# Optimization experiments

Measured on AMD Instinct MI355X. Metric: run time of the kernel, lower is better.

## Reference

```python
import jax, jax.numpy as jnp
import numpy as np

T, B, I, H, O = 256, 64, 512, 1024, 256


def setup_inputs() -> dict:
    key = jax.random.key(0)
    ks = jax.random.split(key, 7)
    s_ih = 1.0 / np.sqrt(H)
    return {
        "x": jax.random.normal(ks[0], (T, B, I), dtype=jnp.float32),
        "W_ih": jax.random.uniform(ks[1], (4 * H, I), dtype=jnp.float32, minval=-s_ih, maxval=s_ih),
        "W_hh": jax.random.uniform(ks[2], (4 * H, H), dtype=jnp.float32, minval=-s_ih, maxval=s_ih),
        "b_ih": jax.random.uniform(ks[3], (4 * H,), dtype=jnp.float32, minval=-s_ih, maxval=s_ih),
        "b_hh": jax.random.uniform(ks[4], (4 * H,), dtype=jnp.float32, minval=-s_ih, maxval=s_ih),
        "fc_W": jax.random.uniform(ks[5], (O, H), dtype=jnp.float32, minval=-s_ih, maxval=s_ih),
        "fc_b": jax.random.uniform(ks[6], (O,), dtype=jnp.float32, minval=-s_ih, maxval=s_ih),
    }


def _lstm(x, W_ih, W_hh, b_ih, b_hh):
    # x: (T, B, I) seq-first, as PyTorch default. Gate order: i, f, g, o.
    Bsz = x.shape[1]
    Hh = W_hh.shape[1]
    # precompute input projections for all time steps: (T, B, 4H)
    xz = jnp.einsum('tbi,gi->tbg', x, W_ih) + b_ih + b_hh

    def step(carry, xz_t):
        h, c = carry
        z = xz_t + h @ W_hh.T  # (B, 4H)
        i, f, g, o = jnp.split(z, 4, axis=-1)
        i = jax.nn.sigmoid(i)
        f = jax.nn.sigmoid(f)
        g = jnp.tanh(g)
        o = jax.nn.sigmoid(o)
        c = f * c + i * g
        h = o * jnp.tanh(c)
        return (h, c), h

    h0 = jnp.zeros((Bsz, Hh), dtype=x.dtype)
    c0 = jnp.zeros((Bsz, Hh), dtype=x.dtype)
    _, hs = jax.lax.scan(step, (h0, c0), xz)
    return hs  # (T, B, H)


def reference(x, W_ih, W_hh, b_ih, b_hh, fc_W, fc_b):
    out = _lstm(x, W_ih, W_hh, b_ih, b_hh)  # (T, B, H)
    # Faithful to original: out[:, -1, :] indexes the LAST BATCH element
    # (seq-first layout), giving (T, H), then fc -> (T, O).
    last = out[:, -1, :]
    return last @ fc_W.T + fc_b
```

## Files before the change

kernel.cpp:

```cpp
#include <hip/hip_runtime.h>
#include <hip/hip_bf16.h>
#include <stdint.h>

#define T_STEPS 256
#define BATCH   64
#define IN_DIM  512
#define HID     1024
#define OUT_DIM 256
#define G4      4096
#define SENT32  0x7FC07FC0u
#define SENT64  0x7FC07FC07FC07FC0ULL
#define WSTRIDE 1028

__device__ __forceinline__ float bfbits2f(uint32_t b16) {
    return __uint_as_float(b16 << 16);
}
__device__ __forceinline__ uint32_t f2bfbits(float f) {
    uint32_t u = __float_as_uint(f);
    u += 0x7fffu + ((u >> 16) & 1u);
    return u >> 16;
}
__device__ __forceinline__ float fast_sigmoid(float x) {
    return 1.f / (1.f + __expf(-x));
}
__device__ __forceinline__ float fast_tanh(float x) {
    return 2.f / (1.f + __expf(-2.f * x)) - 1.f;
}
__device__ __forceinline__ bool any_sent(uint64_t v) {
    uint64_t x = v ^ SENT64;
    return (((x - 0x0001000100010001ULL) & ~x) & 0x8000800080008000ULL) != 0ULL;
}
__device__ __forceinline__ uint64_t poll_load(const uint64_t* p) {
    return __hip_atomic_load(p, __ATOMIC_RELAXED, __HIP_MEMORY_SCOPE_AGENT);
}

__global__ void init_sent(uint32_t* __restrict__ p, int n) {
    int i = blockIdx.x * 256 + threadIdx.x;
    if (i < n) p[i] = SENT32;
}

template<bool ABF16>
__global__ __launch_bounds__(256) void gemm_bt(
    const void* __restrict__ Av, long lda,
    const float* __restrict__ Bw, int ldb,
    const float* __restrict__ bias1,
    float* __restrict__ C, int ldc, int K)
{
    __shared__ float a_lds[64][68];
    __shared__ float w_lds[64][65];
    const int tid = threadIdx.x;
    const int m0 = blockIdx.y * 64, n0 = blockIdx.x * 64;
    const int kl = tid & 63, grp = tid >> 6;
    const int cc = tid & 31, r0 = (tid >> 5) * 8;

    float acc[16];
#pragma unroll
    for (int i = 0; i < 16; ++i) acc[i] = 0.f;

    for (int k0 = 0; k0 < K; k0 += 64) {
        __syncthreads();
#pragma unroll
        for (int i = 0; i < 16; ++i) {
            int r = grp + 4 * i;
            long ai = (long)(m0 + r) * lda + k0 + kl;
            float av = ABF16 ? bfbits2f(((const uint16_t*)Av)[ai])
                             : ((const float*)Av)[ai];
            a_lds[kl][r] = av;
            w_lds[kl][r] = Bw[(long)(n0 + r) * ldb + k0 + kl];
        }
        __syncthreads();
#pragma unroll 16
        for (int k = 0; k < 64; ++k) {
            float4 A0 = *(const float4*)&a_lds[k][r0];
            float4 A1 = *(const float4*)&a_lds[k][r0 + 4];
            float w0 = w_lds[k][cc], w1 = w_lds[k][cc + 32];
            float a[8] = {A0.x, A0.y, A0.z, A0.w, A1.x, A1.y, A1.z, A1.w};
#pragma unroll
            for (int i = 0; i < 8; ++i) {
                acc[i]     += a[i] * w0;
                acc[8 + i] += a[i] * w1;
            }
        }
    }
    float b0 = bias1[n0 + cc], b1 = bias1[n0 + cc + 32];
#pragma unroll
    for (int i = 0; i < 8; ++i) {
        C[(long)(m0 + r0 + i) * ldc + n0 + cc]      = acc[i]     + b0;
        C[(long)(m0 + r0 + i) * ldc + n0 + cc + 32] = acc[8 + i] + b1;
    }
}

#define GROWX(RR) ((long)((RR) >> 2) * HID + 4 * g + ((RR) & 3))

__global__ __launch_bounds__(256, 1) void lstm_rec(
    const float* __restrict__ W_hh,
    const float* __restrict__ x,
    const float* __restrict__ W_ih,
    const float* __restrict__ b_ih,
    const float* __restrict__ b_hh,
    uint64_t* __restrict__ h_all)
{
    __shared__ float W_lds[16][WSTRIDE];
    __shared__ float h_lds[2][HID];
    __shared__ float xz_lds[16][T_STEPS + 1];
    __shared__ float z_lds[16];

    const int g   = blockIdx.x;
    const int tid = threadIdx.x;
    const int kpart = tid & 15;
    const int row   = tid >> 4;
    const long grow = GROWX(row);

    {
        const float* wsrc = W_hh + grow * HID;
#pragma unroll
        for (int i = 0; i < 16; ++i) {
            const int col = kpart * 64 + ((i + kpart) & 15) * 4;
            *(float4*)&W_lds[row][col] = *(const float4*)(wsrc + col);
        }
    }

    {
        const int wv = tid >> 6;
        const int ln = tid & 63;
        const int rr0 = 4 * wv;
        const long gr0 = GROWX(rr0), gr1 = GROWX(rr0 + 1),
                   gr2 = GROWX(rr0 + 2), gr3 = GROWX(rr0 + 3);
        const float4 p0a = *(const float4*)(W_ih + gr0 * IN_DIM + 8 * ln);
        const float4 p0b = *(const float4*)(W_ih + gr0 * IN_DIM + 8 * ln + 4);
        const float4 p1a = *(const float4*)(W_ih + gr1 * IN_DIM + 8 * ln);
        const float4 p1b = *(const float4*)(W_ih + gr1 * IN_DIM + 8 * ln + 4);
        const float4 p2a = *(const float4*)(W_ih + gr2 * IN_DIM + 8 * ln);
        const float4 p2b = *(const float4*)(W_ih + gr2 * IN_DIM + 8 * ln + 4);
        const float4 p3a = *(const float4*)(W_ih + gr3 * IN_DIM + 8 * ln);
        const float4 p3b = *(const float4*)(W_ih + gr3 * IN_DIM + 8 * ln + 4);
        const float bs0 = b_ih[gr0] + b_hh[gr0];
        const float bs1 = b_ih[gr1] + b_hh[gr1];
        const float bs2 = b_ih[gr2] + b_hh[gr2];
        const float bs3 = b_ih[gr3] + b_hh[gr3];
        for (int t = 0; t < T_STEPS; ++t) {
            const float* xp = x + ((long)t * BATCH + 63) * IN_DIM + 8 * ln;
            const float4 xa = *(const float4*)xp;
            const float4 xb = *(const float4*)(xp + 4);
            float s0 = xa.x*p0a.x + xa.y*p0a.y + xa.z*p0a.z + xa.w*p0a.w
                     + xb.x*p0b.x + xb.y*p0b.y + xb.z*p0b.z + xb.w*p0b.w;
            float s1 = xa.x*p1a.x + xa.y*p1a.y + xa.z*p1a.z + xa.w*p1a.w
                     + xb.x*p1b.x + xb.y*p1b.y + xb.z*p1b.z + xb.w*p1b.w;
            float s2 = xa.x*p2a.x + xa.y*p2a.y + xa.z*p2a.z + xa.w*p2a.w
                     + xb.x*p2b.x + xb.y*p2b.y + xb.z*p2b.z + xb.w*p2b.w;
            float s3 = xa.x*p3a.x + xa.y*p3a.y + xa.z*p3a.z + xa.w*p3a.w
                     + xb.x*p3b.x + xb.y*p3b.y + xb.z*p3b.z + xb.w*p3b.w;
#pragma unroll
            for (int d = 1; d < 64; d <<= 1) {
                s0 += __shfl_xor(s0, d, 64);
                s1 += __shfl_xor(s1, d, 64);
                s2 += __shfl_xor(s2, d, 64);
                s3 += __shfl_xor(s3, d, 64);
            }
            if (ln == 0) {
                xz_lds[rr0 + 0][t] = s0 + bs0;
                xz_lds[rr0 + 1][t] = s1 + bs1;
                xz_lds[rr0 + 2][t] = s2 + bs2;
                xz_lds[rr0 + 3][t] = s3 + bs3;
            }
        }
    }

    {
        float4 z4 = {0.f, 0.f, 0.f, 0.f};
        *(float4*)&h_lds[0][4 * tid] = z4;
    }
    __syncthreads();

    float c_state = 0.f;
    float xz_next = xz_lds[row][0];

    for (int t = 0; t < T_STEPS; ++t) {
        float* hb = h_lds[t & 1];
        if (t > 0) {
            const uint64_t* src = h_all + (size_t)(t - 1) * 256 + tid;
            uint64_t v  = poll_load(src);
            uint64_t a_ = poll_load(src);
            uint64_t b_ = poll_load(src);
            while (any_sent(v)) {
                v = a_; a_ = b_; b_ = poll_load(src);
            }
            float4 f0 = { bfbits2f((uint32_t)( v        & 0xFFFFu)),
                          bfbits2f((uint32_t)((v >> 16) & 0xFFFFu)),
                          bfbits2f((uint32_t)((v >> 32) & 0xFFFFu)),
                          bfbits2f((uint32_t)((v >> 48) & 0xFFFFu)) };
            *(float4*)&hb[4 * tid] = f0;
        }
        __syncthreads();
        asm volatile("" ::: "memory");

        const float xz_cur = xz_next;
        const int tn = (t + 1 < T_STEPS) ? t + 1 : t;
        xz_next = xz_lds[row][tn];

        float a0 = 0.f, a1 = 0.f, a2 = 0.f, a3 = 0.f;
#pragma unroll
        for (int i = 0; i < 16; ++i) {
            const int col = kpart * 64 + ((i + kpart) & 15) * 4;
            const float4 wv4 = *(const float4*)&W_lds[row][col];
            const float4 hv  = *(const float4*)&hb[col];
            a0 = fmaf(wv4.x, hv.x, a0);
            a1 = fmaf(wv4.y, hv.y, a1);
            a2 = fmaf(wv4.z, hv.z, a2);
            a3 = fmaf(wv4.w, hv.w, a3);
        }
        float sum = (a0 + a1) + (a2 + a3);
        sum += __shfl_xor(sum, 1, 16);
        sum += __shfl_xor(sum, 2, 16);
        sum += __shfl_xor(sum, 4, 16);
        sum += __shfl_xor(sum, 8, 16);
        if (kpart == 0) z_lds[row] = sum + xz_cur;
        __syncthreads();

        if (tid < 4) {
            const float zi = z_lds[tid],     zf = z_lds[4 + tid];
            const float zg = z_lds[8 + tid], zo = z_lds[12 + tid];
            const float ii = fast_sigmoid(zi);
            const float ff = fast_sigmoid(zf);
            const float gg = fast_tanh(zg);
            const float oo = fast_sigmoid(zo);
            c_state = ff * c_state + ii * gg;
            const float h = oo * fast_tanh(c_state);
            uint32_t hbv = f2bfbits(h);
            uint32_t lo  = hbv | (__shfl_down(hbv, 1, 64) << 16);
            uint64_t A   = (uint64_t)lo | ((uint64_t)__shfl(lo, 2, 64) << 32);
            if (tid == 0) {
                __hip_atomic_store(&h_all[(size_t)t * 256 + g], A,
                                   __ATOMIC_RELAXED, __HIP_MEMORY_SCOPE_AGENT);
            }
        }
    }
}

extern "C" void kernel_launch(void* const* d_in, const int* in_sizes, int n_in,
                              void* d_out, int out_size, void* d_ws, size_t ws_size,
                              hipStream_t stream) {
    const float* x    = (const float*)d_in[0];
    const float* W_ih = (const float*)d_in[1];
    const float* W_hh = (const float*)d_in[2];
    const float* b_ih = (const float*)d_in[3];
    const float* b_hh = (const float*)d_in[4];
    const float* fc_W = (const float*)d_in[5];
    const float* fc_b = (const float*)d_in[6];
    float* out = (float*)d_out;

    uint64_t* h_all = (uint64_t*)d_ws;

    init_sent<<<512, 256, 0, stream>>>((uint32_t*)h_all, T_STEPS * HID / 2);

    lstm_rec<<<256, 256, 0, stream>>>(W_hh, x, W_ih, b_ih, b_hh, h_all);

    gemm_bt<true><<<dim3(OUT_DIM / 64, T_STEPS / 64), 256, 0, stream>>>(
        (const void*)h_all, HID, fc_W, HID, fc_b, out, OUT_DIM, HID);
}
```

Before: 1.163 ms.

## Replace sentinel polling with striped release/acquire step counters

Each of the 256 blocks publishes its h slice and then atomically increments one of eight per-step counters, each padded onto its own cache line, with release semantics. Consumers have eight threads spin on these counters with acquire loads, then read h once after a block barrier. This replaces every thread polling its own h word for NaN sentinels, which cuts polling traffic. In exchange it adds an atomic RMW chain per step and an extra barrier, which may lengthen the critical path of the recurrence.

Result: slower. 3.101 ms (+166.6%).

```diff
diff --git a/kernel.cpp b/kernel.cpp
--- a/kernel.cpp
+++ b/kernel.cpp
@@ -8,8 +8,6 @@
 #define HID     1024
 #define OUT_DIM 256
 #define G4      4096
-#define SENT32  0x7FC07FC0u
-#define SENT64  0x7FC07FC07FC07FC0ULL
 #define WSTRIDE 1028
 
 __device__ __forceinline__ float bfbits2f(uint32_t b16) {
@@ -26,17 +24,10 @@
 __device__ __forceinline__ float fast_tanh(float x) {
     return 2.f / (1.f + __expf(-2.f * x)) - 1.f;
 }
-__device__ __forceinline__ bool any_sent(uint64_t v) {
-    uint64_t x = v ^ SENT64;
-    return (((x - 0x0001000100010001ULL) & ~x) & 0x8000800080008000ULL) != 0ULL;
-}
-__device__ __forceinline__ uint64_t poll_load(const uint64_t* p) {
-    return __hip_atomic_load(p, __ATOMIC_RELAXED, __HIP_MEMORY_SCOPE_AGENT);
-}
-
-__global__ void init_sent(uint32_t* __restrict__ p, int n) {
+
+__global__ void init_zero(uint32_t* __restrict__ p, int n) {
     int i = blockIdx.x * 256 + threadIdx.x;
-    if (i < n) p[i] = SENT32;
+    if (i < n) p[i] = 0u;
 }
 
 template<bool ABF16>
@@ -98,7 +89,8 @@
     const float* __restrict__ W_ih,
     const float* __restrict__ b_ih,
     const float* __restrict__ b_hh,
-    uint64_t* __restrict__ h_all)
+    uint64_t* __restrict__ h_all,
+    uint32_t* __restrict__ cnt)
 {
     __shared__ float W_lds[16][WSTRIDE];
     __shared__ float h_lds[2][HID];
@@ -178,13 +170,15 @@
     for (int t = 0; t < T_STEPS; ++t) {
         float* hb = h_lds[t & 1];
         if (t > 0) {
-            const uint64_t* src = h_all + (size_t)(t - 1) * 256 + tid;
-            uint64_t v  = poll_load(src);
-            uint64_t a_ = poll_load(src);
-            uint64_t b_ = poll_load(src);
-            while (any_sent(v)) {
-                v = a_; a_ = b_; b_ = poll_load(src);
-            }
+            if (tid < 8) {
+                const uint32_t* cp = cnt + ((size_t)(t - 1) * 8 + tid) * 64;
+                while (__hip_atomic_load(cp, __ATOMIC_ACQUIRE,
+                                         __HIP_MEMORY_SCOPE_AGENT) != 32u) {}
+            }
+            __syncthreads();
+            const uint64_t v = __hip_atomic_load(
+                &h_all[(size_t)(t - 1) * 256 + tid],
+                __ATOMIC_RELAXED, __HIP_MEMORY_SCOPE_AGENT);
             float4 f0 = { bfbits2f((uint32_t)( v        & 0xFFFFu)),
                           bfbits2f((uint32_t)((v >> 16) & 0xFFFFu)),
                           bfbits2f((uint32_t)((v >> 32) & 0xFFFFu)),
@@ -232,6 +226,8 @@
             if (tid == 0) {
                 __hip_atomic_store(&h_all[(size_t)t * 256 + g], A,
                                    __ATOMIC_RELAXED, __HIP_MEMORY_SCOPE_AGENT);
+                __hip_atomic_fetch_add(&cnt[((size_t)t * 8 + (g & 7)) * 64], 1u,
+                                       __ATOMIC_RELEASE, __HIP_MEMORY_SCOPE_AGENT);
             }
         }
     }
@@ -250,10 +246,11 @@
     float* out = (float*)d_out;
 
     uint64_t* h_all = (uint64_t*)d_ws;
-
-    init_sent<<<512, 256, 0, stream>>>((uint32_t*)h_all, T_STEPS * HID / 2);
-
-    lstm_rec<<<256, 256, 0, stream>>>(W_hh, x, W_ih, b_ih, b_hh, h_all);
+    uint32_t* cnt   = (uint32_t*)((char*)d_ws + 512 * 1024);
+
+    init_zero<<<512, 256, 0, stream>>>(cnt, T_STEPS * 8 * 64);
+
+    lstm_rec<<<256, 256, 0, stream>>>(W_hh, x, W_ih, b_ih, b_hh, h_all, cnt);
 
     gemm_bt<true><<<dim3(OUT_DIM / 64, T_STEPS / 64), 256, 0, stream>>>(
         (const void*)h_all, HID, fc_W, HID, fc_b, out, OUT_DIM, HID);
```
